# Kernel tuning notes

Measured on AMD Instinct MI355X. Metric: run time of the kernel, lower is better.

The kernel has to match this reference:

```python
import jax, jax.numpy as jnp
import numpy as np

D = 4          # guide-feature dimension (in_channels_feature)
NV = D + 1     # simplex vertices / lattice remainders
BASE = 128     # per-coordinate key encoding base
OFF = 64
SENT = np.int32(2 ** 30)  # sentinel hash for unused slots


def _elevation_matrix(d):
    # Adams et al. elevation: cf = f * scale; elevated = E @ cf, built densely.
    E = np.zeros((d + 1, d), np.float32)
    E[0, :] = 1.0
    for i in range(1, d + 1):
        E[i, i - 1] = -i
        E[i, i:] = 1.0
    scale = 1.0 / np.sqrt((np.arange(d) + 1.0) * (np.arange(d) + 2.0))
    scale = scale * (d + 1.0) * np.sqrt(2.0 / 3.0)  # inv_std_dev
    return (E * scale[None, :]).astype(np.float32)


def _neighbor_offsets(d):
    # lattice axis vectors u_j (first d coords): u_j[i] = d if i==j else -1
    U = -np.ones((d + 1, d), np.int64)
    for j in range(d):
        U[j, j] = d
    offs = []
    for m in range(2 ** (d + 1) - 1):  # all subsets of axes except the full set
        c = [(m >> j) & 1 for j in range(d + 1)]
        offs.append(sum(c[j] * U[j] for j in range(d + 1)))
    return np.stack(offs).astype(np.int32)  # (F, d), F = 2^(d+1)-1


_EMB = jnp.asarray(_elevation_matrix(D))          # (NV, D)
_OFFS = jnp.asarray(_neighbor_offsets(D))         # (F, D)
_POW = jnp.asarray((BASE ** np.arange(D)).astype(np.int32))


def _encode(keys):  # (..., D) int32 -> (...,) int32 perfect hash within range
    k = jnp.clip(keys, -OFF, OFF - 1) + OFF
    return (k * _POW).sum(-1)


def _lattice_filter(feat, dat, Wk):
    # feat: (N, D) guide features; dat: (N, Cin); Wk: (Cout, Cin, F)
    N = feat.shape[0]
    M0 = N * NV  # max distinct lattice points
    elev = feat @ _EMB.T                      # (N, NV)
    g = jnp.round(elev / NV) * NV             # nearest remainder-0 point
    gi = jnp.round(g).astype(jnp.int32)
    s = gi.sum(-1) // NV                      # exact: coords are multiples of NV
    diff = elev - g
    order = jnp.argsort(-diff, axis=-1)       # stable descending sort of residuals
    rank = jnp.argsort(order, axis=-1).astype(jnp.int32) + s[:, None]
    low, high = rank < 0, rank > D
    rank = jnp.where(low, rank + NV, jnp.where(high, rank - NV, rank))
    gi = jnp.where(low, gi + NV, jnp.where(high, gi - NV, gi))
    t = (elev - gi.astype(elev.dtype)) / NV
    rows = jnp.arange(N)[:, None]
    bary = jnp.zeros((N, D + 2), elev.dtype)
    bary = bary.at[rows, D - rank].add(t)
    bary = bary.at[rows, NV - rank].add(1.0 - t)
    bary = bary.at[:, 0].add(1.0 + bary[:, D + 1])
    bary = bary[:, :NV]                       # (N, NV) barycentric weights
    # simplex vertex keys, first D coords only (last is -sum)
    kk = jnp.arange(NV, dtype=jnp.int32)[None, :, None]       # vertex color
    add = jnp.where(rank[:, None, :D] >= NV - kk, kk - NV, kk)
    keys = gi[:, None, :D] + add              # (N, NV, D)
    codes = _encode(keys)                     # (N, NV)
    # --- dedup lattice points (sort + first-occurrence ranks) ---
    flat = codes.reshape(-1)
    sortv = jnp.sort(flat)
    is_new = jnp.concatenate([jnp.ones((1,), bool), sortv[1:] != sortv[:-1]])
    urank = jnp.cumsum(is_new) - 1
    uniq = jnp.full((M0,), SENT, jnp.int32).at[urank].set(sortv)  # sorted uniques
    idx = jnp.searchsorted(uniq, flat)        # (M0,) slot of each (point,vertex)
    # --- splat ---
    Cin = dat.shape[1]
    vals = (dat[:, None, :] * bary[:, :, None]).reshape(M0, Cin)
    table = jnp.zeros((M0, Cin), dat.dtype).at[idx].add(vals)
    ukeys = jnp.zeros((M0, D), jnp.int32).at[idx].set(keys.reshape(M0, D))
    # --- blur: learned conv over lattice neighborhood ---
    ncodes = _encode(ukeys[:, None, :] + _OFFS[None, :, :])   # (M0, F)
    pos = jnp.clip(jnp.searchsorted(uniq, ncodes), 0, M0 - 1)
    valid = (uniq[pos] == ncodes)[..., None]
    gathered = table[pos] * valid             # (M0, F, Cin)
    out_lat = jnp.einsum('mfc,ocf->mo', gathered, Wk)  # (M0, Cout)
    # --- slice ---
    out = jnp.einsum('nk,nko->no', bary, out_lat[idx.reshape(N, NV)])
    return out  # (N, Cout)


def setup_inputs() -> dict:
    key = jax.random.key(0)
    k1, k2, k3, k4 = jax.random.split(key, 4)
    B, Cin, Cout, H, W = 4, 64, 64, 32, 32
    F = 2 ** (D + 1) - 1  # 31 = get_filter_size(1, D)
    return {
        'data': jax.random.normal(k1, (B, Cin, H, W), jnp.float32),
        'features': jax.random.normal(k2, (B, D, H, W), jnp.float32),
        'weights': 0.02 * jax.random.normal(k3, (Cout, Cin, 1, F), jnp.float32),
        'bias': 0.1 * jax.random.normal(k4, (1, 1, 1, Cout), jnp.float32),
        'bias_multiplier': jnp.ones((1, 1, 1, H * W), jnp.float32),
    }


def reference(data, features, weights, bias, bias_multiplier):
    B, Cin, H, W = data.shape
    N = H * W
    feat = features.reshape(B, D, N).transpose(0, 2, 1)   # (B, N, D)
    dat = data.reshape(B, Cin, N).transpose(0, 2, 1)      # (B, N, Cin)
    Wk = weights[:, :, 0, :]                              # (Cout, Cin, F)
    out = jax.vmap(lambda f, x: _lattice_filter(f, x, Wk))(feat, dat)  # (B, N, Cout)
    out = out + bias.reshape(-1)[None, None, :] * bias_multiplier.reshape(-1)[None, :, None]
    Cout = Wk.shape[0]
    return out.transpose(0, 2, 1).reshape(B, Cout, H, W)
```

## Files before the change

kernel.cpp:

```cpp
#include <hip/hip_runtime.h>
#include <hip/hip_bf16.h>
#include <stdint.h>

#define DD 4
#define NVERT 5
#define NPTS 1024
#define BATCH 4
#define M0 5120
#define CIN 64
#define COUT 64
#define NF 31
#define KTOT 1984
#define CAP 16384
#define CAPMASK (CAP-1)
#define SENTV 1073741824
#define ZROW (BATCH*M0)

using bf16x8 = __attribute__((ext_vector_type(8))) short;
using f32x4  = __attribute__((ext_vector_type(4))) float;

__device__ __forceinline__ unsigned short f2bf(float x){
  unsigned int u = __float_as_uint(x);
  u = (u + 0x7FFFu + ((u >> 16) & 1u)) >> 16;
  return (unsigned short)u;
}

__device__ __forceinline__ uint32_t hslot(int code){
  return (((uint32_t)code * 2654435761u) >> 18) & CAPMASK;
}

__device__ __forceinline__ void pv_math(const float* feat, int g, int* code_out, float* bary_out){
  int p = g / NVERT, kk = g % NVERT;
  int b = p >> 10, n = p & 1023;
  const float* fb = feat + (size_t)b * DD * NPTS + n;
  float f0 = fb[0], f1 = fb[NPTS], f2 = fb[2 * NPTS], f3 = fb[3 * NPTS];

  float elev[5];
  elev[0] =  f0 * 2.886751345948129f  + f1 * 1.6666666666666667f + f2 * 1.1785113019775793f + f3 * 0.9128709291752769f;
  elev[1] = -f0 * 2.886751345948129f  + f1 * 1.6666666666666667f + f2 * 1.1785113019775793f + f3 * 0.9128709291752769f;
  elev[2] =  f1 * -3.3333333333333335f + f2 * 1.1785113019775793f + f3 * 0.9128709291752769f;
  elev[3] =  f2 * -3.535533905932738f  + f3 * 0.9128709291752769f;
  elev[4] =  f3 * -3.6514837167011076f;

  int gi[5]; float diff[5]; int sum = 0;
  #pragma unroll
  for (int i = 0; i < 5; i++){
    float gg = rintf(elev[i] * 0.2f) * 5.0f;
    gi[i] = (int)rintf(gg);
    sum += gi[i];
    diff[i] = elev[i] - gg;
  }
  int s = sum / 5;

  int rank[5];
  #pragma unroll
  for (int i = 0; i < 5; i++){
    int r = 0;
    #pragma unroll
    for (int j = 0; j < 5; j++)
      r += (diff[j] > diff[i]) || (diff[j] == diff[i] && j < i);
    rank[i] = r + s;
  }
  #pragma unroll
  for (int i = 0; i < 5; i++){
    if (rank[i] < 0)      { rank[i] += NVERT; gi[i] += NVERT; }
    else if (rank[i] > DD){ rank[i] -= NVERT; gi[i] -= NVERT; }
  }

  float bary[6] = {0.f,0.f,0.f,0.f,0.f,0.f};
  #pragma unroll
  for (int i = 0; i < 5; i++){
    float tt = (elev[i] - (float)gi[i]) * 0.2f;
    bary[DD - rank[i]]    += tt;
    bary[NVERT - rank[i]] += 1.0f - tt;
  }
  bary[0] += 1.0f + bary[5];

  float bk = bary[0];
  #pragma unroll
  for (int i = 1; i < 5; i++) if (i == kk) bk = bary[i];

  int code = 0;
  #pragma unroll
  for (int j = 0; j < DD; j++){
    int add = (rank[j] >= NVERT - kk) ? (kk - NVERT) : kk;
    int key = gi[j] + add;
    key = min(63, max(-64, key));
    code += (key + 64) << (7 * j);
  }
  *code_out = code;
  *bary_out = bk;
}

__global__ void k_a(const float* __restrict__ wk, const float* __restrict__ data,
                    const float* __restrict__ feat,
                    int* __restrict__ hc, int* __restrict__ hu, int* __restrict__ uc,
                    float4* __restrict__ table4, unsigned short* __restrict__ bpf,
                    float* __restrict__ dat_t,
                    int* __restrict__ codes_pv, float* __restrict__ bary_pv){
  int bid = blockIdx.x, tid = threadIdx.x;
  if (bid < 64){
    __shared__ float tile[64][65];
    int b = bid >> 4, n0 = (bid & 15) * 64;
    int nl = tid & 63;
    #pragma unroll
    for (int i = 0; i < 16; i++){
      int c = (tid >> 6) * 16 + i;
      tile[c][nl] = data[(((size_t)b * 64 + c) << 10) + n0 + nl];
    }
    __syncthreads();
    #pragma unroll
    for (int i = 0; i < 16; i++){
      int nn = (tid >> 6) * 16 + i;
      dat_t[(((size_t)b << 10) + n0 + nn) * 64 + (tid & 63)] = tile[tid & 63][nn];
    }
  } else if (bid < 144){
    int g = (bid - 64) * 256 + tid;
    int code; float bk;
    pv_math(feat, g, &code, &bk);
    codes_pv[g] = code;
    bary_pv[g]  = bk;
  } else if (bid < 640){
    int e = (bid - 144) * 256 + tid;
    int frag = e >> 9, l = (e >> 3) & 63, j = e & 7;
    int f = frag >> 3, h = (frag >> 2) & 1, g = frag & 3;
    int col = g * 16 + (l & 15);
    int c = h * 32 + ((l >> 4) << 3) + j;
    bpf[e] = f2bf(wk[(col * CIN + c) * NF + f]);
  } else {
    int g = (bid - 640) * 256 + tid;
    int stride = 384 * 256;
    for (int i = g; i < BATCH * CAP; i += stride){ hc[i] = SENTV; hu[i] = -1; }
    if (g < BATCH) uc[g] = 0;
    float4 z = {0.f,0.f,0.f,0.f};
    for (int i = g; i < BATCH * M0 * CIN / 4; i += stride) table4[i] = z;
  }
}

__global__ void k_insert(const int* __restrict__ codes_pv,
                         int* __restrict__ hash_code, int* __restrict__ hash_uid,
                         int* __restrict__ ucount, int* __restrict__ ukeys){
  __shared__ int lhash[512];
  int tid = threadIdx.x;
  lhash[tid] = SENTV; lhash[tid + 256] = SENTV;
  __syncthreads();

  int g = blockIdx.x * 256 + tid;
  int b = g / M0;
  int code = codes_pv[g];

  uint32_t lh = (((uint32_t)code * 2654435761u) >> 21) & 511;
  bool rep = false;
  while (true){
    int prev = atomicCAS(&lhash[lh], SENTV, code);
    if (prev == SENTV){ rep = true; break; }
    if (prev == code) break;
    lh = (lh + 1) & 511;
  }

  int myslot = -1;
  if (rep){
    int* hc = hash_code + b * CAP;
    uint32_t h = hslot(code);
    while (true){
      int prev = atomicCAS(&hc[h], SENTV, code);
      if (prev == SENTV){ myslot = (int)h; break; }
      if (prev == code) break;
      h = (h + 1) & CAPMASK;
    }
  }

  unsigned long long mask = __ballot(myslot >= 0);
  if (mask){
    int lane = tid & 63;
    int cnt = __popcll(mask);
    int leader = __ffsll((unsigned long long)mask) - 1;
    int base = 0;
    if (lane == leader) base = atomicAdd(&ucount[b], cnt);
    base = __shfl(base, leader);
    if (myslot >= 0){
      int rank = __popcll(mask & ((1ull << lane) - 1ull));
      int uid = base + rank;
      hash_uid[b * CAP + myslot] = uid;
      int* uk = ukeys + ((size_t)(b * M0 + uid)) * DD;
      #pragma unroll
      for (int j = 0; j < DD; j++) uk[j] = ((code >> (7 * j)) & 127) - 64;
    }
  }
}

__global__ void k_sn(const float* __restrict__ dat_t, const int* __restrict__ codes_pv,
                     const float* __restrict__ bary_pv, const int* __restrict__ hash_code,
                     const int* __restrict__ hash_uid, const int* __restrict__ ucount,
                     const int* __restrict__ ukeys,
                     int* __restrict__ idx_pv, float* __restrict__ table,
                     int* __restrict__ nuid){
  int bid = blockIdx.x, tid = threadIdx.x;
  if (bid < BATCH * NPTS / 4){
    __shared__ int   us[4][8];
    __shared__ float wbs[4][8];
    int w = tid >> 6, lane = tid & 63;
    int p = bid * 4 + w;
    int b = p >> 10;
    float v = dat_t[((size_t)p << 6) + lane];
    if (lane < NVERT){
      int code = codes_pv[p * NVERT + lane];
      const int* hc = hash_code + b * CAP;
      uint32_t h = hslot(code);
      while (hc[h] != code) h = (h + 1) & CAPMASK;
      int uid = hash_uid[b * CAP + h];
      us[w][lane]  = uid;
      wbs[w][lane] = bary_pv[p * NVERT + lane];
      idx_pv[p * NVERT + lane] = uid;
    }
    __syncthreads();
    int rot = p % NVERT;
    #pragma unroll
    for (int kq = 0; kq < NVERT; kq++){
      int kk = kq + rot; if (kk >= NVERT) kk -= NVERT;
      atomicAdd(&table[(((size_t)(b * M0 + us[w][kk])) << 6) + lane], v * wbs[w][kk]);
    }
  } else {
    int e = (bid - BATCH * NPTS / 4) * 256 + tid;
    int f = e & 31;
    int idx = e >> 5;
    int b = idx / M0, m = idx - b * M0;
    int g = ZROW;
    if (f < NF && m < ucount[b]){
      const int* uk = ukeys + ((size_t)idx) * DD;
      int pc = __popc(f);
      int code = 0;
      #pragma unroll
      for (int j = 0; j < DD; j++){
        int key = uk[j] + 5 * ((f >> j) & 1) - pc;
        key = min(63, max(-64, key));
        code += (key + 64) << (7 * j);
      }
      const int* hc = hash_code + b * CAP;
      uint32_t h = hslot(code);
      while (true){
        int v = hc[h];
        if (v == code){ g = b * M0 + hash_uid[b * CAP + h]; break; }
        if (v == SENTV) break;
        h = (h + 1) & CAPMASK;
      }
    }
    nuid[e] = g;
  }
}

__global__ void k_tobf(const float* __restrict__ table, unsigned short* __restrict__ table_bf){
  int g = blockIdx.x * blockDim.x + threadIdx.x;
  size_t base = (size_t)g * 8;
  const float4* s4 = (const float4*)(table + base);
  float4 x = s4[0], y = s4[1];
  bf16x8 v;
  v[0] = (short)f2bf(x.x); v[1] = (short)f2bf(x.y);
  v[2] = (short)f2bf(x.z); v[3] = (short)f2bf(x.w);
  v[4] = (short)f2bf(y.x); v[5] = (short)f2bf(y.y);
  v[6] = (short)f2bf(y.z); v[7] = (short)f2bf(y.w);
  *(bf16x8*)(table_bf + base) = v;
  if (g < 8){
    bf16x8 z = {0,0,0,0,0,0,0,0};
    *(bf16x8*)(table_bf + ((size_t)ZROW << 6) + g * 8) = z;
  }
}

__launch_bounds__(512, 4)
__global__ void k_conv(const int* __restrict__ ucount, const int* __restrict__ nuid,
                       const unsigned short* __restrict__ table_bf,
                       const unsigned short* __restrict__ bpf,
                       float* __restrict__ out_lat){
  __shared__ int gidx_s[64 * 33];
  __shared__ float red[3][2][64][33];

  int blk = blockIdx.x;
  int b   = blk / (M0 / 64);
  int m0  = (blk % (M0 / 64)) * 64;
  if (m0 >= ucount[b]) return;

  int tid = threadIdx.x;
  {
    int base = (b * M0 + m0) << 5;
    #pragma unroll
    for (int i = 0; i < 4; i++){
      int idx = tid + i * 512;
      gidx_s[(idx >> 5) * 33 + (idx & 31)] = nuid[base + idx];
    }
  }
  __syncthreads();

  int lane = tid & 63, wave = tid >> 6;
  int wm = wave & 1, wk = wave >> 1;
  int arow = wm * 32 + (lane & 15);
  int acol = (lane >> 4) * 8;
  const unsigned short* bf_lane = bpf + ((size_t)lane << 3);

  f32x4 acc0[4], acc1[4];
  #pragma unroll
  for (int g = 0; g < 4; g++){
    acc0[g] = (f32x4){0.f,0.f,0.f,0.f};
    acc1[g] = (f32x4){0.f,0.f,0.f,0.f};
  }

  const int kfs[5] = {0, 8, 16, 24, 31};
  int f0 = kfs[wk], f1 = kfs[wk + 1], flast = f1 - 1;

  const unsigned short* r0p = table_bf + (((size_t)gidx_s[arow * 33 + f0]) << 6) + acol;
  const unsigned short* r1p = table_bf + (((size_t)gidx_s[(arow + 16) * 33 + f0]) << 6) + acol;
  bf16x8 A00 = *(const bf16x8*)(r0p);
  bf16x8 A01 = *(const bf16x8*)(r0p + 32);
  bf16x8 A10 = *(const bf16x8*)(r1p);
  bf16x8 A11 = *(const bf16x8*)(r1p + 32);

  #pragma unroll 2
  for (int f = f0; f < f1; f++){
    bf16x8 c00 = A00, c01 = A01, c10 = A10, c11 = A11;
    int fn = f + 1 > flast ? flast : f + 1;
    const unsigned short* n0p = table_bf + (((size_t)gidx_s[arow * 33 + fn]) << 6) + acol;
    const unsigned short* n1p = table_bf + (((size_t)gidx_s[(arow + 16) * 33 + fn]) << 6) + acol;
    A00 = *(const bf16x8*)(n0p);
    A01 = *(const bf16x8*)(n0p + 32);
    A10 = *(const bf16x8*)(n1p);
    A11 = *(const bf16x8*)(n1p + 32);

    int fr = f << 3;
    #pragma unroll
    for (int g = 0; g < 4; g++){
      bf16x8 B0 = *(const bf16x8*)(bf_lane + ((size_t)(fr + g)     << 9));
      bf16x8 B1 = *(const bf16x8*)(bf_lane + ((size_t)(fr + 4 + g) << 9));
      acc0[g] = __builtin_amdgcn_mfma_f32_16x16x32_bf16(c00, B0, acc0[g], 0, 0, 0);
      acc0[g] = __builtin_amdgcn_mfma_f32_16x16x32_bf16(c01, B1, acc0[g], 0, 0, 0);
      acc1[g] = __builtin_amdgcn_mfma_f32_16x16x32_bf16(c10, B0, acc1[g], 0, 0, 0);
      acc1[g] = __builtin_amdgcn_mfma_f32_16x16x32_bf16(c11, B1, acc1[g], 0, 0, 0);
    }
  }

  if (wk > 0){
    #pragma unroll
    for (int g = 0; g < 4; g++){
      #pragma unroll
      for (int q = 0; q < 4; q++){
        red[wk - 1][wm][lane][g * 4 + q]      = acc0[g][q];
        red[wk - 1][wm][lane][16 + g * 4 + q] = acc1[g][q];
      }
    }
  }
  __syncthreads();
  if (wk == 0){
    #pragma unroll
    for (int r = 0; r < 3; r++){
      #pragma unroll
      for (int g = 0; g < 4; g++){
        #pragma unroll
        for (int q = 0; q < 4; q++){
          acc0[g][q] += red[r][wm][lane][g * 4 + q];
          acc1[g][q] += red[r][wm][lane][16 + g * 4 + q];
        }
      }
    }
    int q4 = (lane >> 4) * 4, col = lane & 15;
    #pragma unroll
    for (int i = 0; i < 2; i++){
      #pragma unroll
      for (int q = 0; q < 4; q++){
        int m = m0 + wm * 32 + i * 16 + q4 + q;
        float* orow = out_lat + (((size_t)(b * M0 + m)) << 6);
        #pragma unroll
        for (int g = 0; g < 4; g++){
          orow[g * 16 + col] = (i == 0) ? acc0[g][q] : acc1[g][q];
        }
      }
    }
  }
}

__global__ void k_slice(const float* __restrict__ bary_pv, const int* __restrict__ idx_pv,
                        const float* __restrict__ out_lat, const float* __restrict__ bias,
                        const float* __restrict__ bmul, float* __restrict__ out){
  __shared__ float tile[32][65];
  int b = blockIdx.x >> 5, n0 = (blockIdx.x & 31) * 32;
  int tid = threadIdx.x;
  int wave = tid >> 6, o = tid & 63;
  float bo = bias[o];
  #pragma unroll
  for (int i = 0; i < 8; i++){
    int n = wave * 8 + i;
    int p = (b << 10) + n0 + n;
    float acc = bo * bmul[n0 + n];
    int base = p * NVERT;
    #pragma unroll
    for (int kk = 0; kk < NVERT; kk++){
      int u = idx_pv[base + kk];
      acc += bary_pv[base + kk] * out_lat[(((size_t)(b * M0 + u)) << 6) + o];
    }
    tile[n][o] = acc;
  }
  __syncthreads();
  int nl = tid & 31, ob = (tid >> 5) * 8;
  #pragma unroll
  for (int i = 0; i < 8; i++){
    int o2 = ob + i;
    out[(((size_t)b * 64 + o2) << 10) + n0 + nl] = tile[nl][o2];
  }
}

extern "C" void kernel_launch(void* const* d_in, const int* in_sizes, int n_in,
                              void* d_out, int out_size, void* d_ws, size_t ws_size,
                              hipStream_t stream){
  const float* data = (const float*)d_in[0];
  const float* feat = (const float*)d_in[1];
  const float* wk   = (const float*)d_in[2];
  const float* bias = (const float*)d_in[3];
  const float* bmul = (const float*)d_in[4];
  float* out = (float*)d_out;

  char* ws = (char*)d_ws;
  size_t off = 0;
  auto alloc = [&](size_t bytes){
    void* p = ws + off;
    off = (off + bytes + 255) & ~(size_t)255;
    return p;
  };
  int*   codes_pv = (int*)  alloc((size_t)BATCH * M0 * 4);
  float* bary_pv  = (float*)alloc((size_t)BATCH * M0 * 4);
  int*   idx_pv   = (int*)  alloc((size_t)BATCH * M0 * 4);
  int*   hash_code= (int*)  alloc((size_t)BATCH * CAP * 4);
  int*   hash_uid = (int*)  alloc((size_t)BATCH * CAP * 4);
  int*   ucount   = (int*)  alloc(256);
  int*   ukeys    = (int*)  alloc((size_t)BATCH * M0 * DD * 4);
  float* table    = (float*)alloc((size_t)BATCH * M0 * CIN * 4);
  float* out_lat  = (float*)alloc((size_t)BATCH * M0 * COUT * 4);
  unsigned short* bpf      = (unsigned short*)alloc((size_t)COUT * KTOT * 2);
  unsigned short* table_bf = (unsigned short*)alloc(((size_t)BATCH * M0 + 8) * CIN * 2);
  float* dat_t    = (float*)alloc((size_t)BATCH * NPTS * CIN * 4);
  int*   nuid     = (int*)  alloc((size_t)BATCH * M0 * 32 * 4);

  k_a     <<<1024, 256, 0, stream>>>(wk, data, feat, hash_code, hash_uid, ucount,
                                     (float4*)table, bpf, dat_t, codes_pv, bary_pv);
  k_insert<<<BATCH * M0 / 256, 256, 0, stream>>>(codes_pv, hash_code, hash_uid, ucount, ukeys);
  k_sn    <<<BATCH * NPTS / 4 + BATCH * M0 * 32 / 256, 256, 0, stream>>>(
            dat_t, codes_pv, bary_pv, hash_code, hash_uid, ucount, ukeys,
            idx_pv, table, nuid);
  k_tobf  <<<BATCH * M0 * CIN / 8 / 256, 256, 0, stream>>>(table, table_bf);
  k_conv  <<<BATCH * (M0 / 64), 512, 0, stream>>>(ucount, nuid, table_bf, bpf, out_lat);
  k_slice <<<BATCH * 32, 256, 0, stream>>>(bary_pv, idx_pv, out_lat, bias, bmul, out);
}
```

Before: 48.31 us.

## Split conv filter taps across two blocks with atomic accumulation; halve slice tile

The lattice convolution now splits its 31 filter taps across two blocks per 64-row tile, each wave handling about 4 taps, and accumulates partial results into out_lat with float atomicAdd. This replaces the shared-memory cross-wave reduction and doubles the number of conv blocks to raise parallelism on a small grid. out_lat must now be zeroed in the setup kernel, which adds memory writes, and the atomic adds make the summation order nondeterministic. The slice kernel is also retiled to 16 points per block, doubling its block count.

```diff
diff --git a/kernel.cpp b/kernel.cpp
--- a/kernel.cpp
+++ b/kernel.cpp
@@ -95,8 +95,8 @@
 __global__ void k_a(const float* __restrict__ wk, const float* __restrict__ data,
                     const float* __restrict__ feat,
                     int* __restrict__ hc, int* __restrict__ hu, int* __restrict__ uc,
-                    float4* __restrict__ table4, unsigned short* __restrict__ bpf,
-                    float* __restrict__ dat_t,
+                    float4* __restrict__ table4, float4* __restrict__ outlat4,
+                    unsigned short* __restrict__ bpf, float* __restrict__ dat_t,
                     int* __restrict__ codes_pv, float* __restrict__ bary_pv){
   int bid = blockIdx.x, tid = threadIdx.x;
   if (bid < 64){
@@ -134,6 +134,7 @@
     if (g < BATCH) uc[g] = 0;
     float4 z = {0.f,0.f,0.f,0.f};
     for (int i = g; i < BATCH * M0 * CIN / 4; i += stride) table4[i] = z;
+    for (int i = g; i < BATCH * M0 * COUT / 4; i += stride) outlat4[i] = z;
   }
 }
 
@@ -272,11 +273,12 @@
                        const unsigned short* __restrict__ bpf,
                        float* __restrict__ out_lat){
   __shared__ int gidx_s[64 * 33];
-  __shared__ float red[3][2][64][33];
 
   int blk = blockIdx.x;
-  int b   = blk / (M0 / 64);
-  int m0  = (blk % (M0 / 64)) * 64;
+  int b    = blk / 160;
+  int r    = blk % 160;
+  int m0   = (r >> 1) * 64;
+  int half = r & 1;
   if (m0 >= ucount[b]) return;
 
   int tid = threadIdx.x;
@@ -303,8 +305,8 @@
     acc1[g] = (f32x4){0.f,0.f,0.f,0.f};
   }
 
-  const int kfs[5] = {0, 8, 16, 24, 31};
-  int f0 = kfs[wk], f1 = kfs[wk + 1], flast = f1 - 1;
+  const int kfsA[2][5] = {{0,4,8,12,16},{16,20,24,28,31}};
+  int f0 = kfsA[half][wk], f1 = kfsA[half][wk + 1], flast = f1 - 1;
 
   const unsigned short* r0p = table_bf + (((size_t)gidx_s[arow * 33 + f0]) << 6) + acol;
   const unsigned short* r1p = table_bf + (((size_t)gidx_s[(arow + 16) * 33 + f0]) << 6) + acol;
@@ -336,40 +338,16 @@
     }
   }
 
-  if (wk > 0){
-    #pragma unroll
-    for (int g = 0; g < 4; g++){
-      #pragma unroll
-      for (int q = 0; q < 4; q++){
-        red[wk - 1][wm][lane][g * 4 + q]      = acc0[g][q];
-        red[wk - 1][wm][lane][16 + g * 4 + q] = acc1[g][q];
-      }
-    }
-  }
-  __syncthreads();
-  if (wk == 0){
-    #pragma unroll
-    for (int r = 0; r < 3; r++){
+  int q4 = (lane >> 4) * 4, col = lane & 15;
+  #pragma unroll
+  for (int i = 0; i < 2; i++){
+    #pragma unroll
+    for (int q = 0; q < 4; q++){
+      int m = m0 + wm * 32 + i * 16 + q4 + q;
+      float* orow = out_lat + (((size_t)(b * M0 + m)) << 6);
       #pragma unroll
       for (int g = 0; g < 4; g++){
-        #pragma unroll
-        for (int q = 0; q < 4; q++){
-          acc0[g][q] += red[r][wm][lane][g * 4 + q];
-          acc1[g][q] += red[r][wm][lane][16 + g * 4 + q];
-        }
-      }
-    }
-    int q4 = (lane >> 4) * 4, col = lane & 15;
-    #pragma unroll
-    for (int i = 0; i < 2; i++){
-      #pragma unroll
-      for (int q = 0; q < 4; q++){
-        int m = m0 + wm * 32 + i * 16 + q4 + q;
-        float* orow = out_lat + (((size_t)(b * M0 + m)) << 6);
-        #pragma unroll
-        for (int g = 0; g < 4; g++){
-          orow[g * 16 + col] = (i == 0) ? acc0[g][q] : acc1[g][q];
-        }
+        atomicAdd(&orow[g * 16 + col], (i == 0) ? acc0[g][q] : acc1[g][q]);
       }
     }
   }
@@ -378,14 +356,14 @@
 __global__ void k_slice(const float* __restrict__ bary_pv, const int* __restrict__ idx_pv,
                         const float* __restrict__ out_lat, const float* __restrict__ bias,
                         const float* __restrict__ bmul, float* __restrict__ out){
-  __shared__ float tile[32][65];
-  int b = blockIdx.x >> 5, n0 = (blockIdx.x & 31) * 32;
+  __shared__ float tile[16][65];
+  int b = blockIdx.x >> 6, n0 = (blockIdx.x & 63) * 16;
   int tid = threadIdx.x;
   int wave = tid >> 6, o = tid & 63;
   float bo = bias[o];
   #pragma unroll
-  for (int i = 0; i < 8; i++){
-    int n = wave * 8 + i;
+  for (int i = 0; i < 4; i++){
+    int n = wave * 4 + i;
     int p = (b << 10) + n0 + n;
     float acc = bo * bmul[n0 + n];
     int base = p * NVERT;
@@ -397,10 +375,10 @@
     tile[n][o] = acc;
   }
   __syncthreads();
-  int nl = tid & 31, ob = (tid >> 5) * 8;
-  #pragma unroll
-  for (int i = 0; i < 8; i++){
-    int o2 = ob + i;
+  int nl = tid & 15;
+  #pragma unroll
+  for (int i = 0; i < 4; i++){
+    int o2 = (tid >> 4) + i * 16;
     out[(((size_t)b * 64 + o2) << 10) + n0 + nl] = tile[nl][o2];
   }
 }
@@ -437,12 +415,13 @@
   int*   nuid     = (int*)  alloc((size_t)BATCH * M0 * 32 * 4);
 
   k_a     <<<1024, 256, 0, stream>>>(wk, data, feat, hash_code, hash_uid, ucount,
-                                     (float4*)table, bpf, dat_t, codes_pv, bary_pv);
+                                     (float4*)table, (float4*)out_lat, bpf, dat_t,
+                                     codes_pv, bary_pv);
   k_insert<<<BATCH * M0 / 256, 256, 0, stream>>>(codes_pv, hash_code, hash_uid, ucount, ukeys);
   k_sn    <<<BATCH * NPTS / 4 + BATCH * M0 * 32 / 256, 256, 0, stream>>>(
             dat_t, codes_pv, bary_pv, hash_code, hash_uid, ucount, ukeys,
             idx_pv, table, nuid);
   k_tobf  <<<BATCH * M0 * CIN / 8 / 256, 256, 0, stream>>>(table, table_bf);
-  k_conv  <<<BATCH * (M0 / 64), 512, 0, stream>>>(ucount, nuid, table_bf, bpf, out_lat);
-  k_slice <<<BATCH * 32, 256, 0, stream>>>(bary_pv, idx_pv, out_lat, bias, bmul, out);
-}
+  k_conv  <<<BATCH * 160, 512, 0, stream>>>(ucount, nuid, table_bf, bpf, out_lat);
+  k_slice <<<BATCH * 64, 256, 0, stream>>>(bary_pv, idx_pv, out_lat, bias, bmul, out);
+}
```

Result: faster. 46.74 us (-3.3%).
